# Kernel optimization log

Measured on AMD Instinct MI355X. Metric: run time of the kernel, lower is better.

Reference implementation:

```python
import jax, jax.numpy as jnp
import numpy as np

E, T, D = 100000, 400000, 128
LN_EPS = 1e-5


def setup_inputs() -> dict:
    key = jax.random.key(0)
    k1, k2, k3 = jax.random.split(key, 3)
    f_edge = jax.random.normal(k1, (E, D), dtype=jnp.float32)
    W = jax.random.normal(k2, (3 * D, D), dtype=jnp.float32) / np.sqrt(3 * D)
    b = jnp.zeros((D,), dtype=jnp.float32)
    gamma = jnp.ones((D,), dtype=jnp.float32)
    beta = jnp.zeros((D,), dtype=jnp.float32)
    triangle = jax.random.randint(k3, (T, 3), 0, E, dtype=jnp.int64)
    return {"f_edge": f_edge, "W": W, "b": b, "gamma": gamma, "beta": beta,
            "triangle": triangle}


def reference(f_edge, W, b, gamma, beta, triangle):
    # f_edge [E, D], triangle [T, 3] -> gather to [T, 3, D], flatten to [T, 3D]
    t = triangle.shape[0]
    e, d = f_edge.shape
    f_tri = f_edge[triangle].reshape(t, 3 * d)
    # Linear(3D -> D) + exact GELU (torch nn.GELU default is erf-based)
    h = jax.nn.gelu(f_tri @ W + b, approximate=False)  # [T, D]
    # scatter_mean over destination edge index triangle[:, 2], dim_size=E
    dst = triangle[:, 2]
    seg_sum = jax.ops.segment_sum(h, dst, num_segments=e)            # [E, D]
    cnt = jax.ops.segment_sum(jnp.ones((t,), h.dtype), dst, num_segments=e)
    mean = seg_sum / jnp.maximum(cnt, 1.0)[:, None]
    # dropout is identity in eval mode; LayerNorm over last dim
    mu = jnp.mean(mean, axis=-1, keepdims=True)
    var = jnp.mean(jnp.square(mean - mu), axis=-1, keepdims=True)
    return (mean - mu) / jnp.sqrt(var + LN_EPS) * gamma + beta
```

## Files before the change

### kernel.cpp

```cpp
#include <hip/hip_runtime.h>
#include <hip/hip_bf16.h>

typedef __attribute__((ext_vector_type(8))) short short8;
typedef __attribute__((ext_vector_type(4))) float floatx4;
typedef __attribute__((ext_vector_type(4))) unsigned int uintx4;

__device__ __forceinline__ float gelu_fast(float x)
{
    float u = 0.7978845608f * x * (1.0f + 0.044715f * x * x);
    float e = __builtin_amdgcn_exp2f(2.885390082f * u);
    return x - x * __builtin_amdgcn_rcpf(e + 1.0f);
}

__global__ __launch_bounds__(256)
void prep(const float* __restrict__ Wg, uintx4* __restrict__ wq,
          const int* __restrict__ tri, int* __restrict__ cnt,
          int* __restrict__ slot, int T)
{
    int g = blockIdx.x * 256 + threadIdx.x;
    if (g < T) {
        int i2 = tri[g * 3 + 2];
        slot[g] = atomicAdd(&cnt[i2], 1);
    } else {
        int i = g - T;
        if (i < 6144) {
            int frag = i >> 6, lane = i & 63;
            int ko = frag >> 3, nt = frag & 7;
            int col = lane & 15, quad = lane >> 4;
            unsigned short tmp[8] __attribute__((aligned(16)));
#pragma unroll
            for (int j = 0; j < 8; ++j) {
                __hip_bfloat16 b =
                    __float2bfloat16(Wg[(ko * 32 + quad * 8 + j) * 128 + nt * 16 + col]);
                tmp[j] = *(unsigned short*)&b;
            }
            wq[i] = *(const uintx4*)tmp;
        }
    }
}

__device__ __forceinline__ int wave_incl_scan(int v, int lane)
{
#pragma unroll
    for (int o = 1; o < 64; o <<= 1) {
        int u = __shfl_up(v, o);
        if (lane >= o) v += u;
    }
    return v;
}

__global__ __launch_bounds__(1024)
void scan_blk(const int* __restrict__ in, int* __restrict__ outExcl,
              int* __restrict__ partial, int n)
{
    __shared__ int ws[16];
    int t = threadIdx.x;
    int g = blockIdx.x * 1024 + t;
    int lane = t & 63, wv = t >> 6;
    int v = (g < n) ? in[g] : 0;
    int sc = wave_incl_scan(v, lane);
    if (lane == 63) ws[wv] = sc;
    __syncthreads();
    if (wv == 0) {
        int b = (lane < 16) ? ws[lane] : 0;
        int bs = wave_incl_scan(b, lane);
        if (lane < 16) ws[lane] = bs;
    }
    __syncthreads();
    int off = wv ? ws[wv - 1] : 0;
    if (g < n) outExcl[g] = off + sc - v;
    if (partial && t == 0) partial[blockIdx.x] = ws[15];
}

__global__ __launch_bounds__(256)
void scatter(const int* __restrict__ tri, const int* __restrict__ slot,
             const int* __restrict__ excl, const int* __restrict__ pscan,
             const int* __restrict__ cnt, int2* __restrict__ srec,
             int2* __restrict__ rowinfo, int E, int T)
{
    int g = blockIdx.x * 256 + threadIdx.x;
    if (g < T) {
        int i0 = tri[g * 3 + 0];
        int i1 = tri[g * 3 + 1];
        int i2 = tri[g * 3 + 2];
        int pos = excl[i2] + pscan[i2 >> 10] + slot[g];
        srec[pos] = make_int2(i0 << 8, i1 << 8);
    }
    if (g < E)
        rowinfo[g] = make_int2(excl[g] + pscan[g >> 10], cnt[g]);
}

__global__ __launch_bounds__(1024, 1)
void edge_gemm(const float* __restrict__ fe_f, const uintx4* __restrict__ wq,
               unsigned short* __restrict__ G, int E)
{
    __shared__ uintx4 ldsW[6144];

    const int tid  = threadIdx.x;
    const int wv   = tid >> 6;
    const int lane = tid & 63;
    const int col  = lane & 15;
    const int quad = lane >> 4;
    const int ntiles = (E + 15) >> 4;

    for (int i = tid; i < 6144; i += 1024) ldsW[i] = wq[i];
    __syncthreads();

#pragma unroll 1
    for (int tile = blockIdx.x * 16 + wv; tile < ntiles; tile += gridDim.x * 16) {
        int row_a = tile * 16 + col;
        if (row_a >= E) row_a = E - 1;
        const float* arow = fe_f + (size_t)row_a * 128 + quad * 8;

        floatx4 f[8];
#pragma unroll
        for (int l = 0; l < 8; ++l)
            f[l] = *(const floatx4*)(arow + (l >> 1) * 32 + (l & 1) * 4);

        short8 a[4];
#pragma unroll
        for (int ko = 0; ko < 4; ++ko) {
            unsigned short tmp[8] __attribute__((aligned(16)));
#pragma unroll
            for (int j = 0; j < 8; ++j) {
                __hip_bfloat16 b = __float2bfloat16(f[ko * 2 + (j >> 2)][j & 3]);
                tmp[j] = *(unsigned short*)&b;
            }
            a[ko] = *(const short8*)tmp;
        }

#pragma unroll 1
        for (int r = 0; r < 3; ++r) {
            floatx4 acc[8];
#pragma unroll
            for (int nt = 0; nt < 8; ++nt) acc[nt] = (floatx4)0.0f;

#pragma unroll
            for (int ko = 0; ko < 4; ++ko) {
#pragma unroll
                for (int nt = 0; nt < 8; ++nt) {
                    short8 bf = *(const short8*)&ldsW[r * 2048 + (ko * 8 + nt) * 64 + lane];
                    acc[nt] = __builtin_amdgcn_mfma_f32_16x16x32_bf16(a[ko], bf, acc[nt], 0, 0, 0);
                }
            }

            unsigned short* Gr = G + (size_t)r * E * 128;
#pragma unroll
            for (int rr = 0; rr < 4; ++rr) {
                int row = tile * 16 + quad * 4 + rr;
                if (row < E) {
                    unsigned short pk[8] __attribute__((aligned(16)));
#pragma unroll
                    for (int nt = 0; nt < 8; ++nt) {
                        __hip_bfloat16 hb = __float2bfloat16(acc[nt][rr]);
                        pk[nt] = *(unsigned short*)&hb;
                    }
                    *(uintx4*)(Gr + (size_t)row * 128 + col * 8) = *(const uintx4*)pk;
                }
            }
        }
    }
}

__global__ __launch_bounds__(256)
void mean_ln(const unsigned short* __restrict__ G, const int2* __restrict__ rowinfo,
             const int2* __restrict__ srec, const float* __restrict__ bias,
             const float* __restrict__ gamma, const float* __restrict__ beta,
             float* __restrict__ out, int E)
{
    int lane = threadIdx.x & 63;
    int row  = blockIdx.x * 4 + (threadIdx.x >> 6);
    if (row >= E) return;
    int col = lane & 15, q = lane >> 4;
    int boff = (col << 4) + (q << 2);
    const char* g0 = (const char*)G + boff;
    const char* g1 = g0 + (size_t)E * 256;
    const char* g2 = g1 + (size_t)E * 256;
    int j0 = q * 32 + col, j1 = j0 + 16;

    int2 ri = rowinfo[row];
    int s = ri.x, c = ri.y;

    unsigned int w2 = *(const unsigned int*)(g2 + (size_t)row * 256);
    float base0 = __uint_as_float(w2 << 16) + bias[j0];
    float base1 = __uint_as_float(w2 & 0xffff0000u) + bias[j1];

    float x0 = 0.0f, x1 = 0.0f;
    for (int p0 = 0; p0 < c; p0 += 64) {
        int nav = min(64, c - p0);
        int2 rr = srec[s + p0 + (lane < nav ? lane : 0)];
        int p = 0;
        for (; p + 4 < nav; p += 8) {
            int n8 = min(8, nav - p);
            unsigned int w0[8], w1[8];
#pragma unroll
            for (int j = 0; j < 8; ++j) {
                int kk = p + (j < n8 ? j : 0);
                int o0 = __shfl(rr.x, kk);
                int o1 = __shfl(rr.y, kk);
                w0[j] = *(const unsigned int*)(g0 + (size_t)(unsigned)o0);
                w1[j] = *(const unsigned int*)(g1 + (size_t)(unsigned)o1);
            }
#pragma unroll
            for (int j = 0; j < 8; ++j) {
                if (j < n8) {
                    float s0 = __uint_as_float(w0[j] << 16)
                             + __uint_as_float(w1[j] << 16) + base0;
                    float s1 = __uint_as_float(w0[j] & 0xffff0000u)
                             + __uint_as_float(w1[j] & 0xffff0000u) + base1;
                    x0 += gelu_fast(s0);
                    x1 += gelu_fast(s1);
                }
            }
        }
        if (p < nav) {
            int n4 = nav - p;
            unsigned int w0[4], w1[4];
#pragma unroll
            for (int j = 0; j < 4; ++j) {
                int kk = p + (j < n4 ? j : 0);
                int o0 = __shfl(rr.x, kk);
                int o1 = __shfl(rr.y, kk);
                w0[j] = *(const unsigned int*)(g0 + (size_t)(unsigned)o0);
                w1[j] = *(const unsigned int*)(g1 + (size_t)(unsigned)o1);
            }
#pragma unroll
            for (int j = 0; j < 4; ++j) {
                if (j < n4) {
                    float s0 = __uint_as_float(w0[j] << 16)
                             + __uint_as_float(w1[j] << 16) + base0;
                    float s1 = __uint_as_float(w0[j] & 0xffff0000u)
                             + __uint_as_float(w1[j] & 0xffff0000u) + base1;
                    x0 += gelu_fast(s0);
                    x1 += gelu_fast(s1);
                }
            }
        }
    }

    float gm0 = gamma[j0], gm1 = gamma[j1];
    float bt0 = beta[j0],  bt1 = beta[j1];

    float inv = 1.0f / fmaxf((float)c, 1.0f);
    float m0 = x0 * inv, m1 = x1 * inv;
    float sm = m0 + m1;
#pragma unroll
    for (int o = 32; o > 0; o >>= 1) sm += __shfl_xor(sm, o);
    float mu = sm * (1.0f / 128.0f);
    float d0 = m0 - mu, d1 = m1 - mu;
    float v = d0 * d0 + d1 * d1;
#pragma unroll
    for (int o = 32; o > 0; o >>= 1) v += __shfl_xor(v, o);
    float rstd = rsqrtf(v * (1.0f / 128.0f) + 1e-5f);
    __builtin_nontemporal_store(d0 * rstd * gm0 + bt0, &out[(size_t)row * 128 + j0]);
    __builtin_nontemporal_store(d1 * rstd * gm1 + bt1, &out[(size_t)row * 128 + j1]);
}

extern "C" void kernel_launch(void* const* d_in, const int* in_sizes, int n_in,
                              void* d_out, int out_size, void* d_ws, size_t ws_size,
                              hipStream_t stream)
{
    const float* fe_f  = (const float*)d_in[0];
    const float* Wg    = (const float*)d_in[1];
    const float* bias  = (const float*)d_in[2];
    const float* gamma = (const float*)d_in[3];
    const float* beta  = (const float*)d_in[4];
    const int*   tri   = (const int*)d_in[5];

    int E = in_sizes[0] / 128;
    int T = in_sizes[5] / 3;

    unsigned short* G = (unsigned short*)d_ws;
    int2* srec = (int2*)((char*)d_ws + (size_t)3 * E * 256);
    uintx4* wq = (uintx4*)(srec + T + 8);
    int* slot = (int*)(wq + 6144);
    int* cnt  = slot + T;
    int* excl = cnt + E;
    int* partial = excl + E;
    int* pscan = partial + 1024;
    int2* rowinfo = (int2*)(pscan + 1024);

    hipMemsetAsync(cnt, 0, (size_t)E * sizeof(int), stream);

    int total = T + 6144;
    prep<<<(total + 255) / 256, 256, 0, stream>>>(Wg, wq, tri, cnt, slot, T);

    int NB = (E + 1023) / 1024;
    scan_blk<<<NB, 1024, 0, stream>>>(cnt, excl, partial, E);
    scan_blk<<<1, 1024, 0, stream>>>(partial, pscan, nullptr, NB);

    scatter<<<(T + 255) / 256, 256, 0, stream>>>(tri, slot, excl, pscan, cnt,
                                                 srec, rowinfo, E, T);

    edge_gemm<<<256, 1024, 0, stream>>>(fe_f, wq, G, E);

    mean_ln<<<(E + 3) / 4, 256, 0, stream>>>(G, rowinfo, srec, bias, gamma, beta,
                                             (float*)d_out, E);
}
```

Measured before the change: 233.5 us.

## Pack first four triangle records and row header into per-edge padded slots

```diff
diff --git a/kernel.cpp b/kernel.cpp
--- a/kernel.cpp
+++ b/kernel.cpp
@@ -76,18 +76,29 @@
 void scatter(const int* __restrict__ tri, const int* __restrict__ slot,
              const int* __restrict__ excl, const int* __restrict__ pscan,
              const int* __restrict__ cnt, int2* __restrict__ srec,
-             int2* __restrict__ rowinfo, int E, int T)
+             int2* __restrict__ srec_pad, int T)
 {
     int g = blockIdx.x * 256 + threadIdx.x;
-    if (g < T) {
-        int i0 = tri[g * 3 + 0];
-        int i1 = tri[g * 3 + 1];
-        int i2 = tri[g * 3 + 2];
-        int pos = excl[i2] + pscan[i2 >> 10] + slot[g];
-        srec[pos] = make_int2(i0 << 8, i1 << 8);
-    }
-    if (g < E)
-        rowinfo[g] = make_int2(excl[g] + pscan[g >> 10], cnt[g]);
+    if (g >= T) return;
+    int i0 = tri[g * 3 + 0];
+    int i1 = tri[g * 3 + 1];
+    int i2 = tri[g * 3 + 2];
+    int sl = slot[g];
+    int start = excl[i2] + pscan[i2 >> 10];
+    int2 rv = make_int2(i0 << 8, i1 << 8);
+    srec[start + sl] = rv;
+    if (sl < 4) {
+        int2 pv = rv;
+        if (sl == 0) {
+            int c = cnt[i2];
+            pv.x |= (c < 255 ? c : 255);
+            pv.y |= start & 0xff;
+        } else if (sl == 1) {
+            pv.x |= (start >> 8) & 0xff;
+            pv.y |= (start >> 16) & 0xff;
+        }
+        srec_pad[(size_t)i2 * 4 + sl] = pv;
+    }
 }
 
 __global__ __launch_bounds__(1024, 1)
@@ -163,14 +174,15 @@
 }
 
 __global__ __launch_bounds__(256)
-void mean_ln(const unsigned short* __restrict__ G, const int2* __restrict__ rowinfo,
-             const int2* __restrict__ srec, const float* __restrict__ bias,
-             const float* __restrict__ gamma, const float* __restrict__ beta,
-             float* __restrict__ out, int E)
+void mean_ln(const unsigned short* __restrict__ G, const int* __restrict__ cnt,
+             const int2* __restrict__ srec, const uintx4* __restrict__ srec_pad,
+             const float* __restrict__ bias, const float* __restrict__ gamma,
+             const float* __restrict__ beta, float* __restrict__ out, int E)
 {
     int lane = threadIdx.x & 63;
     int row  = blockIdx.x * 4 + (threadIdx.x >> 6);
     if (row >= E) return;
+    int urow = __builtin_amdgcn_readfirstlane(row);
     int col = lane & 15, q = lane >> 4;
     int boff = (col << 4) + (q << 2);
     const char* g0 = (const char*)G + boff;
@@ -178,68 +190,90 @@
     const char* g2 = g1 + (size_t)E * 256;
     int j0 = q * 32 + col, j1 = j0 + 16;
 
-    int2 ri = rowinfo[row];
-    int s = ri.x, c = ri.y;
-
-    unsigned int w2 = *(const unsigned int*)(g2 + (size_t)row * 256);
-    float base0 = __uint_as_float(w2 << 16) + bias[j0];
-    float base1 = __uint_as_float(w2 & 0xffff0000u) + bias[j1];
-
-    float x0 = 0.0f, x1 = 0.0f;
-    for (int p0 = 0; p0 < c; p0 += 64) {
-        int nav = min(64, c - p0);
-        int2 rr = srec[s + p0 + (lane < nav ? lane : 0)];
-        int p = 0;
-        for (; p + 4 < nav; p += 8) {
-            int n8 = min(8, nav - p);
-            unsigned int w0[8], w1[8];
-#pragma unroll
-            for (int j = 0; j < 8; ++j) {
-                int kk = p + (j < n8 ? j : 0);
-                int o0 = __shfl(rr.x, kk);
-                int o1 = __shfl(rr.y, kk);
-                w0[j] = *(const unsigned int*)(g0 + (size_t)(unsigned)o0);
-                w1[j] = *(const unsigned int*)(g1 + (size_t)(unsigned)o1);
-            }
-#pragma unroll
-            for (int j = 0; j < 8; ++j) {
-                if (j < n8) {
-                    float s0 = __uint_as_float(w0[j] << 16)
-                             + __uint_as_float(w1[j] << 16) + base0;
-                    float s1 = __uint_as_float(w0[j] & 0xffff0000u)
-                             + __uint_as_float(w1[j] & 0xffff0000u) + base1;
-                    x0 += gelu_fast(s0);
-                    x1 += gelu_fast(s1);
-                }
-            }
-        }
-        if (p < nav) {
-            int n4 = nav - p;
-            unsigned int w0[4], w1[4];
-#pragma unroll
-            for (int j = 0; j < 4; ++j) {
-                int kk = p + (j < n4 ? j : 0);
-                int o0 = __shfl(rr.x, kk);
-                int o1 = __shfl(rr.y, kk);
-                w0[j] = *(const unsigned int*)(g0 + (size_t)(unsigned)o0);
-                w1[j] = *(const unsigned int*)(g1 + (size_t)(unsigned)o1);
-            }
-#pragma unroll
-            for (int j = 0; j < 4; ++j) {
-                if (j < n4) {
-                    float s0 = __uint_as_float(w0[j] << 16)
-                             + __uint_as_float(w1[j] << 16) + base0;
-                    float s1 = __uint_as_float(w0[j] & 0xffff0000u)
-                             + __uint_as_float(w1[j] & 0xffff0000u) + base1;
-                    x0 += gelu_fast(s0);
-                    x1 += gelu_fast(s1);
-                }
-            }
-        }
-    }
-
+    const uintx4* hp = srec_pad + (size_t)urow * 2;
+    uintx4 h0 = hp[0];
+    uintx4 h1 = hp[1];
+    unsigned int w2 = *(const unsigned int*)(g2 + (size_t)urow * 256);
+    float bv0 = bias[j0], bv1 = bias[j1];
     float gm0 = gamma[j0], gm1 = gamma[j1];
     float bt0 = beta[j0],  bt1 = beta[j1];
+
+    int c = (int)(h0[0] & 255u);
+    if (__builtin_expect(c == 255, 0)) c = cnt[urow];
+
+    const unsigned int M = 0xffffff00u;
+    unsigned int a0[4] = { h0[0] & M, h0[2] & M, h1[0] & M, h1[2] & M };
+    unsigned int a1[4] = { h0[1] & M, h0[3] & M, h1[1] & M, h1[3] & M };
+
+    float base0 = __uint_as_float(w2 << 16) + bv0;
+    float base1 = __uint_as_float(w2 & 0xffff0000u) + bv1;
+
+    float x0 = 0.0f, x1 = 0.0f;
+
+    if (c <= 4) {
+        unsigned int w0[4], w1[4];
+#pragma unroll
+        for (int j = 0; j < 4; ++j) {
+            w0[j] = *(const unsigned int*)(g0 + (size_t)a0[j]);
+            w1[j] = *(const unsigned int*)(g1 + (size_t)a1[j]);
+        }
+#pragma unroll
+        for (int j = 0; j < 4; ++j) {
+            bool ok = j < c;
+            float s0 = __uint_as_float(w0[j] << 16)
+                     + __uint_as_float(w1[j] << 16) + base0;
+            float s1 = __uint_as_float(w0[j] & 0xffff0000u)
+                     + __uint_as_float(w1[j] & 0xffff0000u) + base1;
+            x0 += ok ? gelu_fast(s0) : 0.0f;
+            x1 += ok ? gelu_fast(s1) : 0.0f;
+        }
+    } else {
+        int start = (int)((h0[1] & 255u) | ((h0[2] & 255u) << 8)
+                        | ((h0[3] & 255u) << 16));
+        start = __builtin_amdgcn_readfirstlane(start);
+
+        unsigned int w0[4], w1[4];
+#pragma unroll
+        for (int j = 0; j < 4; ++j) {
+            w0[j] = *(const unsigned int*)(g0 + (size_t)a0[j]);
+            w1[j] = *(const unsigned int*)(g1 + (size_t)a1[j]);
+        }
+#pragma unroll
+        for (int j = 0; j < 4; ++j) {
+            float s0 = __uint_as_float(w0[j] << 16)
+                     + __uint_as_float(w1[j] << 16) + base0;
+            float s1 = __uint_as_float(w0[j] & 0xffff0000u)
+                     + __uint_as_float(w1[j] & 0xffff0000u) + base1;
+            x0 += gelu_fast(s0);
+            x1 += gelu_fast(s1);
+        }
+
+        for (int p = 4; p < c; p += 4) {
+            int2 cr[4];
+#pragma unroll
+            for (int j = 0; j < 4; ++j) {
+                int idx = p + j;
+                if (idx > c - 1) idx = c - 1;
+                cr[j] = srec[start + idx];
+            }
+            unsigned int u0[4], u1[4];
+#pragma unroll
+            for (int j = 0; j < 4; ++j) {
+                u0[j] = *(const unsigned int*)(g0 + (size_t)(unsigned)cr[j].x);
+                u1[j] = *(const unsigned int*)(g1 + (size_t)(unsigned)cr[j].y);
+            }
+#pragma unroll
+            for (int j = 0; j < 4; ++j) {
+                bool ok = (p + j) < c;
+                float s0 = __uint_as_float(u0[j] << 16)
+                         + __uint_as_float(u1[j] << 16) + base0;
+                float s1 = __uint_as_float(u0[j] & 0xffff0000u)
+                         + __uint_as_float(u1[j] & 0xffff0000u) + base1;
+                x0 += ok ? gelu_fast(s0) : 0.0f;
+                x1 += ok ? gelu_fast(s1) : 0.0f;
+            }
+        }
+    }
 
     float inv = 1.0f / fmaxf((float)c, 1.0f);
     float m0 = x0 * inv, m1 = x1 * inv;
@@ -252,8 +286,8 @@
 #pragma unroll
     for (int o = 32; o > 0; o >>= 1) v += __shfl_xor(v, o);
     float rstd = rsqrtf(v * (1.0f / 128.0f) + 1e-5f);
-    __builtin_nontemporal_store(d0 * rstd * gm0 + bt0, &out[(size_t)row * 128 + j0]);
-    __builtin_nontemporal_store(d1 * rstd * gm1 + bt1, &out[(size_t)row * 128 + j1]);
+    __builtin_nontemporal_store(d0 * rstd * gm0 + bt0, &out[(size_t)urow * 128 + j0]);
+    __builtin_nontemporal_store(d1 * rstd * gm1 + bt1, &out[(size_t)urow * 128 + j1]);
 }
 
 extern "C" void kernel_launch(void* const* d_in, const int* in_sizes, int n_in,
@@ -270,17 +304,20 @@
     int E = in_sizes[0] / 128;
     int T = in_sizes[5] / 3;
 
-    unsigned short* G = (unsigned short*)d_ws;
-    int2* srec = (int2*)((char*)d_ws + (size_t)3 * E * 256);
-    uintx4* wq = (uintx4*)(srec + T + 8);
-    int* slot = (int*)(wq + 6144);
-    int* cnt  = slot + T;
-    int* excl = cnt + E;
-    int* partial = excl + E;
-    int* pscan = partial + 1024;
-    int2* rowinfo = (int2*)(pscan + 1024);
-
-    hipMemsetAsync(cnt, 0, (size_t)E * sizeof(int), stream);
+    char* base = (char*)d_ws;
+    unsigned short* G = (unsigned short*)base;
+    int* slot    = (int*)base;
+    int* excl    = (int*)(base + (size_t)T * 4);
+    int* partial = (int*)(base + (size_t)T * 4 + (size_t)E * 4);
+    int* pscan   = partial + 1024;
+
+    char* p = base + (size_t)3 * E * 256;
+    int2* srec = (int2*)p;                 p += (size_t)T * 8;
+    int2* srec_pad = (int2*)p;             p += (size_t)E * 32;
+    int* cnt = (int*)p;                    p += (size_t)E * 4;
+    uintx4* wq = (uintx4*)p;
+
+    (void)hipMemsetAsync(srec_pad, 0, (size_t)E * 32 + (size_t)E * 4, stream);
 
     int total = T + 6144;
     prep<<<(total + 255) / 256, 256, 0, stream>>>(Wg, wq, tri, cnt, slot, T);
@@ -290,10 +327,11 @@
     scan_blk<<<1, 1024, 0, stream>>>(partial, pscan, nullptr, NB);
 
     scatter<<<(T + 255) / 256, 256, 0, stream>>>(tri, slot, excl, pscan, cnt,
-                                                 srec, rowinfo, E, T);
+                                                 srec, srec_pad, T);
 
     edge_gemm<<<256, 1024, 0, stream>>>(fe_f, wq, G, E);
 
-    mean_ln<<<(E + 3) / 4, 256, 0, stream>>>(G, rowinfo, srec, bias, gamma, beta,
-                                             (float*)d_out, E);
-}
+    mean_ln<<<(E + 3) / 4, 256, 0, stream>>>(G, cnt, srec,
+                                             (const uintx4*)srec_pad,
+                                             bias, gamma, beta, (float*)d_out, E);
+}
```

After: 232.7 us. About the same (-0.3%).
